# Optimization experiments

Measured on AMD Instinct MI355X. Metric: run time of the kernel, lower is better.

The kernel has to match this reference:

```python
import jax, jax.numpy as jnp
import numpy as np

B, S, D = 8, 2048, 512

def setup_inputs() -> dict:
    key = jax.random.key(0)
    k1, k2 = jax.random.split(key)
    lstm_out = jax.random.normal(k1, (B, S, D), dtype=jnp.float32)
    # xavier_uniform init for [D, D]
    limit = float(np.sqrt(6.0 / (D + D)))
    attention_weights = jax.random.uniform(k2, (D, D), dtype=jnp.float32, minval=-limit, maxval=limit)
    return {"lstm_out": lstm_out, "attention_weights": attention_weights}

def reference(lstm_out, attention_weights):
    # scores[b,i,j] = tanh( (x W) x^T )
    proj = jnp.einsum('bsd,de->bse', lstm_out, attention_weights)          # [B,S,D]
    scores = jnp.tanh(jnp.einsum('bsd,btd->bst', proj, lstm_out))          # [B,S,S]
    attn = jax.nn.softmax(scores, axis=-1)                                 # [B,S,S]
    return jnp.einsum('bst,btd->bsd', attn, lstm_out)                      # [B,S,D]
```

## Files before the change

kernel.cpp:

```cpp
#include <hip/hip_runtime.h>
#include <hip/hip_bf16.h>

typedef __bf16 bf16;
typedef __attribute__((ext_vector_type(4))) __bf16 bf16x4;
typedef __attribute__((ext_vector_type(8))) __bf16 bf16x8;
typedef __attribute__((ext_vector_type(4))) float floatx4;

#define NSLOT 32

__device__ __forceinline__ void gl_lds16(const bf16* g, bf16* l) {
    __builtin_amdgcn_global_load_lds(
        (const __attribute__((address_space(1))) unsigned int*)g,
        (__attribute__((address_space(3))) unsigned int*)l,
        16, 0, 0);
}

__device__ __forceinline__ void swizzle_mn(int& bm, int& bn) {
    int gx = gridDim.x;
    int f  = blockIdx.y * gx + blockIdx.x;
    int st = f >> 3, r = f & 7;
    int mgroups = gx >> 2;
    bm = (st % mgroups) * 4 + (r & 3);
    bn = (st / mgroups) * 2 + (r >> 2);
}

__global__ __launch_bounds__(256) void cast_both(const float* __restrict__ in,
                                                 bf16* __restrict__ outn,
                                                 bf16* __restrict__ outt,
                                                 int R, int C, int B,
                                                 const float* __restrict__ Wm,
                                                 bf16* __restrict__ wt) {
    __shared__ float tile[64][65];
    const int bz = blockIdx.z;
    const int cl = (threadIdx.x & 15) * 4;
    const int rw = threadIdx.x >> 4;

    if (bz == B) {
        if (blockIdx.x >= 8 || blockIdx.y >= 8) return;
        const int r0 = blockIdx.x * 64, c0 = blockIdx.y * 64;
#pragma unroll
        for (int it = 0; it < 4; ++it) {
            const int r = rw + it * 16;
            floatx4 v = *(const floatx4*)&Wm[(long long)(r0 + r) * 512 + c0 + cl];
            tile[r][cl + 0] = v[0]; tile[r][cl + 1] = v[1];
            tile[r][cl + 2] = v[2]; tile[r][cl + 3] = v[3];
        }
        __syncthreads();
#pragma unroll
        for (int it = 0; it < 4; ++it) {
            const int c = rw + it * 16;
            bf16x4 b;
            b[0] = (bf16)tile[cl + 0][c]; b[1] = (bf16)tile[cl + 1][c];
            b[2] = (bf16)tile[cl + 2][c]; b[3] = (bf16)tile[cl + 3][c];
            *(bf16x4*)&wt[(long long)(c0 + c) * 512 + r0 + cl] = b;
        }
        return;
    }

    in   += (long long)bz * R * C;
    outn += (long long)bz * R * C;
    outt += (long long)bz * R * C;
    const int r0 = blockIdx.x * 64, c0 = blockIdx.y * 64;
#pragma unroll
    for (int it = 0; it < 4; ++it) {
        const int r = rw + it * 16;
        floatx4 v = *(const floatx4*)&in[(long long)(r0 + r) * C + c0 + cl];
        bf16x4 b; b[0] = (bf16)v[0]; b[1] = (bf16)v[1]; b[2] = (bf16)v[2]; b[3] = (bf16)v[3];
        *(bf16x4*)&outn[(long long)(r0 + r) * C + c0 + cl] = b;
        tile[r][cl + 0] = v[0]; tile[r][cl + 1] = v[1];
        tile[r][cl + 2] = v[2]; tile[r][cl + 3] = v[3];
    }
    __syncthreads();
#pragma unroll
    for (int it = 0; it < 4; ++it) {
        const int c = rw + it * 16;
        bf16x4 b;
        b[0] = (bf16)tile[cl + 0][c]; b[1] = (bf16)tile[cl + 1][c];
        b[2] = (bf16)tile[cl + 2][c]; b[3] = (bf16)tile[cl + 3][c];
        *(bf16x4*)&outt[(long long)(c0 + c) * R + r0 + cl] = b;
    }
}

__device__ __forceinline__ float fast_tanh(float v) {
    float e = __expf(2.0f * v);
    return 1.0f - 2.0f / (e + 1.0f);
}

template <int MODE, int BN>
__global__ __launch_bounds__(512, 4) void gemm512(const bf16* __restrict__ A,
                                                  const bf16* __restrict__ Bm,
                                                  void* __restrict__ Cout,
                                                  float* __restrict__ rpart,
                                                  int M, int N, int K,
                                                  long long batchA, long long batchB,
                                                  long long batchC, long long batchR) {
    constexpr int NI = (BN == 128) ? 4 : 2;

    const long long bz = blockIdx.z;
    A  += bz * batchA;
    Bm += bz * batchB;

    __shared__ bf16 As[2][256 * 32];
    __shared__ bf16 Bs[2][BN * 32];
    __shared__ float rs[256];

    const int t    = threadIdx.x;
    const int lane = t & 63;
    const int w    = t >> 6;
    const int quad = lane >> 4;
    const int l16  = lane & 15;
    const int wr   = (BN == 128) ? (w >> 1) : w;
    const int wc   = (BN == 128) ? (w & 1) : 0;

    int bm, bn;
    swizzle_mn(bm, bn);
    const int m0 = bm * 256;
    const int n0 = bn * BN;

    floatx4 acc[NI][4] = {};

    const int srow = t >> 2;
    const int sch  = (((t & 3) ^ ((t >> 3) & 3))) * 8;
    const bf16* Abase = A + (long long)(m0 + srow) * K + sch;
    const bf16* Bbase = Bm + (long long)(n0 + srow) * K + sch;
    const long long r128 = 128LL * K;

    const int rdch = (quad ^ ((l16 >> 1) & 3)) * 8;

    if (MODE == 2) {
        if (t < 256) {
            const float* pp = rpart + (bz * batchR + m0 + t) * NSLOT;
            float s = 0.f;
#pragma unroll
            for (int c = 0; c < NSLOT / 4; ++c) {
                float4 p = ((const float4*)pp)[c];
                s += (p.x + p.y) + (p.z + p.w);
            }
            rs[t] = 1.0f / s;
        }
    }

    auto stage = [&](int buf, int k0) {
        gl_lds16(Abase + k0,        &As[buf][t * 8]);
        gl_lds16(Abase + k0 + r128, &As[buf][t * 8 + 4096]);
        if (BN == 128) {
            gl_lds16(Bbase + k0, &Bs[buf][t * 8]);
        } else {
            if (t < 256) gl_lds16(Bbase + k0, &Bs[buf][t * 8]);
        }
    };

    auto compute = [&](int buf) {
        bf16x8 af[NI], bfr[4];
#pragma unroll
        for (int i = 0; i < NI; ++i)
            af[i] = *(const bf16x8*)(&As[buf][(wr * (NI * 16) + i * 16 + l16) * 32 + rdch]);
#pragma unroll
        for (int j = 0; j < 4; ++j)
            bfr[j] = *(const bf16x8*)(&Bs[buf][(wc * 64 + j * 16 + l16) * 32 + rdch]);
#pragma unroll
        for (int i = 0; i < NI; ++i)
#pragma unroll
            for (int j = 0; j < 4; ++j)
                acc[i][j] = __builtin_amdgcn_mfma_f32_16x16x32_bf16(af[i], bfr[j], acc[i][j], 0, 0, 0);
    };

    const int NT = K >> 5;
    stage(0, 0);
    __syncthreads();
    for (int it = 0; it < NT; ++it) {
        const int buf = it & 1;
        if (it + 1 < NT) stage(buf ^ 1, (it + 1) << 5);
        compute(buf);
        __syncthreads();
    }

    if (MODE == 1) {
        bf16* Cg = (bf16*)Cout + bz * batchC;
        const int slot = bn * 2 + wc;
#pragma unroll
        for (int i = 0; i < NI; ++i)
#pragma unroll
            for (int r = 0; r < 4; ++r) {
                long long row = m0 + wr * (NI * 16) + i * 16 + quad * 4 + r;
                float s = 0.f;
#pragma unroll
                for (int j = 0; j < 4; ++j) {
                    float v = __expf(fast_tanh(acc[i][j][r]));
                    s += v;
                    Cg[row * (long long)N + (n0 + wc * 64 + j * 16 + l16)] = (bf16)v;
                }
#pragma unroll
                for (int msk = 1; msk < 16; msk <<= 1) s += __shfl_xor(s, msk);
                if (l16 == 0)
                    rpart[(bz * batchR + row) * NSLOT + slot] = s;
            }
    } else if (MODE == 2) {
        float* Og = (float*)Cout + bz * batchC;
#pragma unroll
        for (int i = 0; i < NI; ++i)
#pragma unroll
            for (int r = 0; r < 4; ++r) {
                int rl = wr * (NI * 16) + i * 16 + quad * 4 + r;
                float inv = rs[rl];
                long long row = m0 + rl;
#pragma unroll
                for (int j = 0; j < 4; ++j)
                    Og[row * (long long)N + (n0 + wc * 64 + j * 16 + l16)] = acc[i][j][r] * inv;
            }
    } else {
        bf16* Cg = (bf16*)Cout + bz * batchC;
#pragma unroll
        for (int i = 0; i < NI; ++i)
#pragma unroll
            for (int r = 0; r < 4; ++r) {
                long long row = m0 + wr * (NI * 16) + i * 16 + quad * 4 + r;
#pragma unroll
                for (int j = 0; j < 4; ++j)
                    Cg[row * (long long)N + (n0 + wc * 64 + j * 16 + l16)] = (bf16)acc[i][j][r];
            }
    }
}

extern "C" void kernel_launch(void* const* d_in, const int* in_sizes, int n_in,
                              void* d_out, int out_size, void* d_ws, size_t ws_size,
                              hipStream_t stream) {
    const int B = 8, S = 2048, D = 512;
    const float* x = (const float*)d_in[0];
    const float* W = (const float*)d_in[1];
    float* out = (float*)d_out;

    const size_t nx = (size_t)B * S * D;
    const size_t nw = (size_t)D * D;

    char* ws = (char*)d_ws;
    auto al = [](size_t v) { return (v + 255) & ~(size_t)255; };
    size_t off = 0;
    bf16* xb = (bf16*)(ws + off); off = al(off + nx * 2);
    bf16* xt = (bf16*)(ws + off); off = al(off + nx * 2);
    bf16* pb = (bf16*)(ws + off); off = al(off + nx * 2);
    bf16* wt = (bf16*)(ws + off); off = al(off + nw * 2);
    float* rpart = (float*)(ws + off); off = al(off + (size_t)B * S * NSLOT * 4);
    bf16* sb = (bf16*)(ws + off);
    const size_t full_need = off + (size_t)B * S * S * 2;
    const bool batched = (ws_size >= full_need);

    { dim3 g(S / 64, D / 64, B + 1); cast_both<<<g, 256, 0, stream>>>(x, xb, xt, S, D, B, W, wt); }

    {
        dim3 g(B * S / 256, D / 64, 1);
        gemm512<0, 64><<<g, 512, 0, stream>>>(xb, wt, (void*)pb, nullptr, B * S, D, D, 0, 0, 0, 0);
    }

    const long long sd = (long long)S * D;
    const long long ss = (long long)S * S;

    if (batched) {
        dim3 g2(S / 256, S / 128, B);
        gemm512<1, 128><<<g2, 512, 0, stream>>>(pb, xb, (void*)sb, rpart, S, S, D, sd, sd, ss, S);
        dim3 g4(S / 256, D / 64, B);
        gemm512<2, 64><<<g4, 512, 0, stream>>>(sb, xt, (void*)out, rpart, S, D, S, ss, sd, sd, S);
    } else {
        for (int b = 0; b < B; ++b) {
            dim3 g2(S / 256, S / 128, 1);
            gemm512<1, 128><<<g2, 512, 0, stream>>>(pb + (size_t)b * sd, xb + (size_t)b * sd,
                                                    (void*)sb, rpart + (size_t)b * S * NSLOT,
                                                    S, S, D, 0, 0, 0, S);
            dim3 g4(S / 256, D / 64, 1);
            gemm512<2, 64><<<g4, 512, 0, stream>>>(sb, xt + (size_t)b * sd,
                                                   (void*)(out + (size_t)b * sd), rpart + (size_t)b * S * NSLOT,
                                                   S, D, S, 0, 0, 0, S);
        }
    }
}
```

Before: 214.1 us.

## Use 256x64 tiles for all GEMMs, raise occupancy, split row-sum inverse kernel

```diff
diff --git a/kernel.cpp b/kernel.cpp
--- a/kernel.cpp
+++ b/kernel.cpp
@@ -81,43 +81,52 @@
     }
 }
 
+__global__ __launch_bounds__(256) void rowsum_inv(const float* __restrict__ rpart,
+                                                  float* __restrict__ rinv, int rows) {
+    const int r = blockIdx.x * 256 + threadIdx.x;
+    if (r >= rows) return;
+    const float4* p = (const float4*)(rpart + (long long)r * NSLOT);
+    float s = 0.f;
+#pragma unroll
+    for (int c = 0; c < NSLOT / 4; ++c) {
+        float4 v = p[c];
+        s += (v.x + v.y) + (v.z + v.w);
+    }
+    rinv[r] = 1.0f / s;
+}
+
 __device__ __forceinline__ float fast_tanh(float v) {
     float e = __expf(2.0f * v);
     return 1.0f - 2.0f / (e + 1.0f);
 }
 
-template <int MODE, int BN>
-__global__ __launch_bounds__(512, 4) void gemm512(const bf16* __restrict__ A,
+template <int MODE>
+__global__ __launch_bounds__(512, 8) void gemm512(const bf16* __restrict__ A,
                                                   const bf16* __restrict__ Bm,
                                                   void* __restrict__ Cout,
                                                   float* __restrict__ rpart,
                                                   int M, int N, int K,
                                                   long long batchA, long long batchB,
                                                   long long batchC, long long batchR) {
-    constexpr int NI = (BN == 128) ? 4 : 2;
-
     const long long bz = blockIdx.z;
     A  += bz * batchA;
     Bm += bz * batchB;
 
     __shared__ bf16 As[2][256 * 32];
-    __shared__ bf16 Bs[2][BN * 32];
-    __shared__ float rs[256];
+    __shared__ bf16 Bs[2][64 * 32];
 
     const int t    = threadIdx.x;
     const int lane = t & 63;
     const int w    = t >> 6;
     const int quad = lane >> 4;
     const int l16  = lane & 15;
-    const int wr   = (BN == 128) ? (w >> 1) : w;
-    const int wc   = (BN == 128) ? (w & 1) : 0;
 
     int bm, bn;
     swizzle_mn(bm, bn);
     const int m0 = bm * 256;
-    const int n0 = bn * BN;
-
-    floatx4 acc[NI][4] = {};
+    const int n0 = bn * 64;
+
+    floatx4 acc[2][4] = {};
 
     const int srow = t >> 2;
     const int sch  = (((t & 3) ^ ((t >> 3) & 3))) * 8;
@@ -127,42 +136,24 @@
 
     const int rdch = (quad ^ ((l16 >> 1) & 3)) * 8;
 
-    if (MODE == 2) {
-        if (t < 256) {
-            const float* pp = rpart + (bz * batchR + m0 + t) * NSLOT;
-            float s = 0.f;
-#pragma unroll
-            for (int c = 0; c < NSLOT / 4; ++c) {
-                float4 p = ((const float4*)pp)[c];
-                s += (p.x + p.y) + (p.z + p.w);
-            }
-            rs[t] = 1.0f / s;
-        }
-    }
-
     auto stage = [&](int buf, int k0) {
         gl_lds16(Abase + k0,        &As[buf][t * 8]);
         gl_lds16(Abase + k0 + r128, &As[buf][t * 8 + 4096]);
-        if (BN == 128) {
-            gl_lds16(Bbase + k0, &Bs[buf][t * 8]);
-        } else {
-            if (t < 256) gl_lds16(Bbase + k0, &Bs[buf][t * 8]);
-        }
+        if (t < 256) gl_lds16(Bbase + k0, &Bs[buf][t * 8]);
     };
 
     auto compute = [&](int buf) {
-        bf16x8 af[NI], bfr[4];
-#pragma unroll
-        for (int i = 0; i < NI; ++i)
-            af[i] = *(const bf16x8*)(&As[buf][(wr * (NI * 16) + i * 16 + l16) * 32 + rdch]);
-#pragma unroll
-        for (int j = 0; j < 4; ++j)
-            bfr[j] = *(const bf16x8*)(&Bs[buf][(wc * 64 + j * 16 + l16) * 32 + rdch]);
-#pragma unroll
-        for (int i = 0; i < NI; ++i)
-#pragma unroll
-            for (int j = 0; j < 4; ++j)
-                acc[i][j] = __builtin_amdgcn_mfma_f32_16x16x32_bf16(af[i], bfr[j], acc[i][j], 0, 0, 0);
+        bf16x8 af0 = *(const bf16x8*)(&As[buf][(w * 32 + l16) * 32 + rdch]);
+        bf16x8 af1 = *(const bf16x8*)(&As[buf][(w * 32 + 16 + l16) * 32 + rdch]);
+#pragma unroll
+        for (int jh = 0; jh < 2; ++jh) {
+            bf16x8 b0 = *(const bf16x8*)(&Bs[buf][(jh * 32 + l16) * 32 + rdch]);
+            bf16x8 b1 = *(const bf16x8*)(&Bs[buf][(jh * 32 + 16 + l16) * 32 + rdch]);
+            acc[0][jh * 2 + 0] = __builtin_amdgcn_mfma_f32_16x16x32_bf16(af0, b0, acc[0][jh * 2 + 0], 0, 0, 0);
+            acc[0][jh * 2 + 1] = __builtin_amdgcn_mfma_f32_16x16x32_bf16(af0, b1, acc[0][jh * 2 + 1], 0, 0, 0);
+            acc[1][jh * 2 + 0] = __builtin_amdgcn_mfma_f32_16x16x32_bf16(af1, b0, acc[1][jh * 2 + 0], 0, 0, 0);
+            acc[1][jh * 2 + 1] = __builtin_amdgcn_mfma_f32_16x16x32_bf16(af1, b1, acc[1][jh * 2 + 1], 0, 0, 0);
+        }
     };
 
     const int NT = K >> 5;
@@ -177,18 +168,18 @@
 
     if (MODE == 1) {
         bf16* Cg = (bf16*)Cout + bz * batchC;
-        const int slot = bn * 2 + wc;
-#pragma unroll
-        for (int i = 0; i < NI; ++i)
+        const int slot = bn;
+#pragma unroll
+        for (int i = 0; i < 2; ++i)
 #pragma unroll
             for (int r = 0; r < 4; ++r) {
-                long long row = m0 + wr * (NI * 16) + i * 16 + quad * 4 + r;
+                long long row = m0 + w * 32 + i * 16 + quad * 4 + r;
                 float s = 0.f;
 #pragma unroll
                 for (int j = 0; j < 4; ++j) {
                     float v = __expf(fast_tanh(acc[i][j][r]));
                     s += v;
-                    Cg[row * (long long)N + (n0 + wc * 64 + j * 16 + l16)] = (bf16)v;
+                    Cg[row * (long long)N + (n0 + j * 16 + l16)] = (bf16)v;
                 }
 #pragma unroll
                 for (int msk = 1; msk < 16; msk <<= 1) s += __shfl_xor(s, msk);
@@ -197,27 +188,28 @@
             }
     } else if (MODE == 2) {
         float* Og = (float*)Cout + bz * batchC;
-#pragma unroll
-        for (int i = 0; i < NI; ++i)
+        const float* rinv = rpart;
+#pragma unroll
+        for (int i = 0; i < 2; ++i)
 #pragma unroll
             for (int r = 0; r < 4; ++r) {
-                int rl = wr * (NI * 16) + i * 16 + quad * 4 + r;
-                float inv = rs[rl];
+                int rl = w * 32 + i * 16 + quad * 4 + r;
+                float inv = rinv[bz * batchR + m0 + rl];
                 long long row = m0 + rl;
 #pragma unroll
                 for (int j = 0; j < 4; ++j)
-                    Og[row * (long long)N + (n0 + wc * 64 + j * 16 + l16)] = acc[i][j][r] * inv;
+                    Og[row * (long long)N + (n0 + j * 16 + l16)] = acc[i][j][r] * inv;
             }
     } else {
         bf16* Cg = (bf16*)Cout + bz * batchC;
 #pragma unroll
-        for (int i = 0; i < NI; ++i)
+        for (int i = 0; i < 2; ++i)
 #pragma unroll
             for (int r = 0; r < 4; ++r) {
-                long long row = m0 + wr * (NI * 16) + i * 16 + quad * 4 + r;
+                long long row = m0 + w * 32 + i * 16 + quad * 4 + r;
 #pragma unroll
                 for (int j = 0; j < 4; ++j)
-                    Cg[row * (long long)N + (n0 + wc * 64 + j * 16 + l16)] = (bf16)acc[i][j][r];
+                    Cg[row * (long long)N + (n0 + j * 16 + l16)] = (bf16)acc[i][j][r];
             }
     }
 }
@@ -241,6 +233,7 @@
     bf16* pb = (bf16*)(ws + off); off = al(off + nx * 2);
     bf16* wt = (bf16*)(ws + off); off = al(off + nw * 2);
     float* rpart = (float*)(ws + off); off = al(off + (size_t)B * S * NSLOT * 4);
+    float* rinv  = (float*)(ws + off); off = al(off + (size_t)B * S * 4);
     bf16* sb = (bf16*)(ws + off);
     const size_t full_need = off + (size_t)B * S * S * 2;
     const bool batched = (ws_size >= full_need);
@@ -249,27 +242,30 @@
 
     {
         dim3 g(B * S / 256, D / 64, 1);
-        gemm512<0, 64><<<g, 512, 0, stream>>>(xb, wt, (void*)pb, nullptr, B * S, D, D, 0, 0, 0, 0);
+        gemm512<0><<<g, 512, 0, stream>>>(xb, wt, (void*)pb, nullptr, B * S, D, D, 0, 0, 0, 0);
     }
 
     const long long sd = (long long)S * D;
     const long long ss = (long long)S * S;
 
     if (batched) {
-        dim3 g2(S / 256, S / 128, B);
-        gemm512<1, 128><<<g2, 512, 0, stream>>>(pb, xb, (void*)sb, rpart, S, S, D, sd, sd, ss, S);
+        dim3 g2(S / 256, S / 64, B);
+        gemm512<1><<<g2, 512, 0, stream>>>(pb, xb, (void*)sb, rpart, S, S, D, sd, sd, ss, S);
+        rowsum_inv<<<dim3(B * S / 256), 256, 0, stream>>>(rpart, rinv, B * S);
         dim3 g4(S / 256, D / 64, B);
-        gemm512<2, 64><<<g4, 512, 0, stream>>>(sb, xt, (void*)out, rpart, S, D, S, ss, sd, sd, S);
+        gemm512<2><<<g4, 512, 0, stream>>>(sb, xt, (void*)out, rinv, S, D, S, ss, sd, sd, S);
     } else {
         for (int b = 0; b < B; ++b) {
-            dim3 g2(S / 256, S / 128, 1);
-            gemm512<1, 128><<<g2, 512, 0, stream>>>(pb + (size_t)b * sd, xb + (size_t)b * sd,
-                                                    (void*)sb, rpart + (size_t)b * S * NSLOT,
-                                                    S, S, D, 0, 0, 0, S);
+            dim3 g2(S / 256, S / 64, 1);
+            gemm512<1><<<g2, 512, 0, stream>>>(pb + (size_t)b * sd, xb + (size_t)b * sd,
+                                               (void*)sb, rpart + (size_t)b * S * NSLOT,
+                                               S, S, D, 0, 0, 0, S);
+            rowsum_inv<<<dim3(S / 256), 256, 0, stream>>>(rpart + (size_t)b * S * NSLOT,
+                                                          rinv + (size_t)b * S, S);
             dim3 g4(S / 256, D / 64, 1);
-            gemm512<2, 64><<<g4, 512, 0, stream>>>(sb, xt + (size_t)b * sd,
-                                                   (void*)(out + (size_t)b * sd), rpart + (size_t)b * S * NSLOT,
-                                                   S, D, S, 0, 0, 0, S);
-        }
-    }
-}
+            gemm512<2><<<g4, 512, 0, stream>>>(sb, xt + (size_t)b * sd,
+                                               (void*)(out + (size_t)b * sd), rinv + (size_t)b * S,
+                                               S, D, S, 0, 0, 0, S);
+        }
+    }
+}
```

Result: slower. 224.5 us (+4.8%).
